# Kernel optimization log

Measured on AMD Instinct MI355X. Metric: run time of the kernel, lower is better.

## Reference

```python
import jax, jax.numpy as jnp
import numpy as np

S, B, DIM = 1024, 4, 768
N_EXPERTS = 8
# hidden_dim = 256 * ceil(int(2*4*dim/3)/256) = 2048 for dim=768
HID = 2048


def setup_inputs() -> dict:
    key = jax.random.key(0)
    ks = jax.random.split(key, 6)
    scale = 0.02
    return {
        "hidden_states": jax.random.normal(ks[0], (S, B, DIM), dtype=jnp.float32),
        "router_w": jax.random.normal(ks[1], (DIM, N_EXPERTS), dtype=jnp.float32) * scale,
        "router_b": jnp.zeros((N_EXPERTS,), dtype=jnp.float32),
        "w1": jax.random.normal(ks[2], (N_EXPERTS, DIM, HID), dtype=jnp.float32) * scale,
        "w2": jax.random.normal(ks[3], (N_EXPERTS, DIM, HID), dtype=jnp.float32) * scale,
        "w3": jax.random.normal(ks[4], (N_EXPERTS, HID, DIM), dtype=jnp.float32) * scale,
    }


def reference(hidden_states, router_w, router_b, w1, w2, w3):
    s, b, h = hidden_states.shape
    # top-1 router
    route = jax.nn.softmax(hidden_states @ router_w + router_b, axis=2)  # [s,b,E]
    max_prob = jnp.max(route, axis=2).reshape(-1, 1)   # [T,1]
    max_ind = jnp.argmax(route, axis=2).reshape(-1)    # [T]
    x = hidden_states.reshape(-1, h)                   # [T,d]

    out = jnp.zeros_like(x)
    # fixed small loop over experts; masked dispatch (tokens not routed to e
    # are zeroed so they contribute nothing)
    for e in range(N_EXPERTS):
        mask = (max_ind == e)[:, None]                 # [T,1]
        xe = jnp.where(mask, x, 0.0)
        oe = (jax.nn.silu(xe @ w1[e]) * (xe @ w2[e])) @ w3[e]
        out = out + jnp.where(mask, oe, 0.0)

    # original stores expert outputs in a bf16 buffer before the prob combine
    out = out.astype(jnp.bfloat16) * max_prob          # bf16 * f32 -> f32
    return out.reshape(s, b, h)
```

## Files before the change

kernel.cpp:

```cpp
#include <hip/hip_runtime.h>


#define T_TOK 4096
#define DIM   768
#define HID   2048
#define NE    8
#define ECAP  1024

#define KB1 24
#define NB1 128
#define KB2 64
#define NB2 48
#define MBC 64

typedef _Float16 f16x8 __attribute__((ext_vector_type(8)));
typedef float    f32x4 __attribute__((ext_vector_type(4)));

#define AS1 __attribute__((address_space(1)))
#define AS3 __attribute__((address_space(3)))

__device__ __forceinline__ void gload_lds16(const _Float16* g, _Float16* l) {
    __builtin_amdgcn_global_load_lds((const AS1 unsigned int*)g,
                                     (AS3 unsigned int*)l, 16, 0, 0);
}

__device__ __forceinline__ float bf16_rne(float v) {
    unsigned u = __float_as_uint(v);
    unsigned r = (u + 0x7fffu + ((u >> 16) & 1u)) & 0xffff0000u;
    return __uint_as_float(r);
}

__device__ __forceinline__ void convert_tile(
    const float* __restrict__ src, _Float16* __restrict__ dst,
    float* Lt, int N, int KBc, int ngrp, int kgrp)
{
    const int t  = threadIdx.x;
    const int c4 = (t & 31) * 4;
    const int r0 = (t >> 5) * 8;
    const float* p = src + (size_t)(kgrp * 64 + r0) * N + ngrp * 128 + c4;
    float4 v[8];
#pragma unroll
    for (int j = 0; j < 8; ++j) v[j] = *(const float4*)(p + (size_t)j * N);
#pragma unroll
    for (int j = 0; j < 8; ++j) {
        float* row = &Lt[(r0 + j) * 130 + c4];
        *(float2*)(row)     = make_float2(v[j].x, v[j].y);
        *(float2*)(row + 2) = make_float2(v[j].z, v[j].w);
    }
    __syncthreads();

    const int l = t & 63, w = t >> 6;
    const int fr = l & 15, fq = l >> 4;
#pragma unroll
    for (int i = 0; i < 4; ++i) {
        const int cell = w * 4 + i;
        const int kbl = cell >> 3, nbl = cell & 7;
        f16x8 h;
#pragma unroll
        for (int j = 0; j < 8; ++j)
            h[j] = (_Float16)Lt[(kbl * 32 + fq * 8 + j) * 130 + nbl * 16 + fr];
        const int nb = ngrp * 8 + nbl, kb = kgrp * 2 + kbl;
        *(f16x8*)(dst + ((size_t)nb * KBc + kb) * 512 + l * 8) = h;
    }
}

__global__ __launch_bounds__(256) void moe_convert_w1_kernel(
    const float* __restrict__ w1, _Float16* __restrict__ w1s)
{
    __shared__ float Lt[64 * 130];
    const int e = blockIdx.x / 192, tile = blockIdx.x % 192;
    convert_tile(w1 + (size_t)e * DIM * HID, w1s + (size_t)e * NB1 * KB1 * 512,
                 Lt, HID, KB1, tile & 15, tile >> 4);
}

__global__ __launch_bounds__(256) void moe_convert_w2_kernel(
    const float* __restrict__ w2, _Float16* __restrict__ w2s)
{
    __shared__ float Lt[64 * 130];
    const int e = blockIdx.x / 192, tile = blockIdx.x % 192;
    convert_tile(w2 + (size_t)e * DIM * HID, w2s + (size_t)e * NB1 * KB1 * 512,
                 Lt, HID, KB1, tile & 15, tile >> 4);
}

__global__ __launch_bounds__(256) void moe_convert_w3_kernel(
    const float* __restrict__ w3, _Float16* __restrict__ w3s)
{
    __shared__ float Lt[64 * 130];
    const int e = blockIdx.x / 192, tile = blockIdx.x % 192;
    convert_tile(w3 + (size_t)e * HID * DIM, w3s + (size_t)e * NB2 * KB2 * 512,
                 Lt, DIM, KB2, tile % 6, tile / 6);
}

__global__ __launch_bounds__(256) void moe_router_kernel(
    const float* __restrict__ X, const float* __restrict__ rw,
    const float* __restrict__ rb, float* __restrict__ probs,
    int* __restrict__ maxind)
{
    const int t = blockIdx.x * 4 + (threadIdx.x >> 6);
    const int l = threadIdx.x & 63;
    const int e = l >> 3;
    const int g = l & 7;
    const float* x = X + (size_t)t * DIM + g * 96;
    const float* w = rw + e;

    double s0 = 0.0, s1 = 0.0;
#pragma unroll
    for (int j4 = 0; j4 < 24; ++j4) {
        const float4 xv = *(const float4*)(x + j4 * 4);
        const int d = (g * 96 + j4 * 4) * NE;
        s0 += (double)xv.x * (double)w[d];
        s1 += (double)xv.y * (double)w[d + NE];
        s0 += (double)xv.z * (double)w[d + 2 * NE];
        s1 += (double)xv.w * (double)w[d + 3 * NE];
    }
    double s = s0 + s1;
    s += __shfl_xor(s, 1, 64);
    s += __shfl_xor(s, 2, 64);
    s += __shfl_xor(s, 4, 64);
    s += (double)rb[e];

    double m = s; int mi = e;
#pragma unroll
    for (int o = 8; o <= 32; o <<= 1) {
        const double om = __shfl_xor(m, o, 64);
        const int   omi = __shfl_xor(mi, o, 64);
        if (om > m || (om == m && omi < mi)) { m = om; mi = omi; }
    }
    float ex = __expf((float)(s - m));
#pragma unroll
    for (int o = 8; o <= 32; o <<= 1) ex += __shfl_xor(ex, o, 64);

    if (l == 0) { probs[t] = 1.0f / ex; maxind[t] = mi; }
}

__global__ __launch_bounds__(256) void moe_lists_kernel(
    const int* __restrict__ maxind, int* __restrict__ counts,
    int* __restrict__ lists)
{
    const int e = blockIdx.x;
    const int tid = threadIdx.x, wid = tid >> 6, lane = tid & 63;
    __shared__ int wsum[4];
    int* dst = lists + e * T_TOK;
    int base = 0;
    for (int t0 = 0; t0 < T_TOK; t0 += 256) {
        const int t = t0 + tid;
        const bool pred = (maxind[t] == e);
        const unsigned long long bal = __ballot(pred);
        const int prefix = __popcll(bal & ((1ull << lane) - 1ull));
        if (lane == 0) wsum[wid] = __popcll(bal);
        __syncthreads();
        int woff = 0;
#pragma unroll
        for (int w2 = 0; w2 < 4; ++w2)
            if (w2 < wid) woff += wsum[w2];
        const int tot = wsum[0] + wsum[1] + wsum[2] + wsum[3];
        if (pred) dst[base + woff + prefix] = t;
        base += tot;
        __syncthreads();
    }
    if (tid == 0) counts[e] = base;
}

__global__ __launch_bounds__(256) void moe_gather_kernel(
    const float* __restrict__ X, const int* __restrict__ lists,
    const int* __restrict__ counts, _Float16* __restrict__ Ag)
{
    const int e = blockIdx.z;
    int cnt = counts[e]; if (cnt > ECAP) cnt = ECAP;
    const int mgrp = blockIdx.y;
    if (mgrp * 64 >= ((cnt + 63) & ~63)) return;
    const int t = threadIdx.x, w = t >> 6, l = t & 63;
    const int mb = mgrp * 4 + w;
    const int m  = mb * 16 + (l & 15);
    const bool valid = (m < cnt);
    const int tok = valid ? lists[e * T_TOK + m] : 0;
    const float* xr = X + (size_t)tok * DIM + (l >> 4) * 8;
#pragma unroll
    for (int i = 0; i < 4; ++i) {
        const int kb = blockIdx.x * 4 + i;
        float4 a = make_float4(0.f, 0.f, 0.f, 0.f), b = a;
        if (valid) {
            a = *(const float4*)(xr + kb * 32);
            b = *(const float4*)(xr + kb * 32 + 4);
        }
        f16x8 h;
        h[0] = (_Float16)a.x; h[1] = (_Float16)a.y; h[2] = (_Float16)a.z; h[3] = (_Float16)a.w;
        h[4] = (_Float16)b.x; h[5] = (_Float16)b.y; h[6] = (_Float16)b.z; h[7] = (_Float16)b.w;
        *(f16x8*)(Ag + ((size_t)(e * MBC + mb) * KB1 + kb) * 512 + l * 8) = h;
    }
}

__global__ __launch_bounds__(256, 4) void moe_gemm1_kernel(
    const _Float16* __restrict__ Ag, const _Float16* __restrict__ w1s,
    const _Float16* __restrict__ w2s, const int* __restrict__ counts,
    _Float16* __restrict__ Hs)
{
    const int e = blockIdx.z;
    int cnt = counts[e]; if (cnt > ECAP) cnt = ECAP;
    const int by = blockIdx.y, bx = blockIdx.x;
    if (by * 128 >= cnt) return;
    const int t = threadIdx.x, w = t >> 6, l = t & 63;
    const int wm = w & 1, wn = w >> 1;

    __shared__ _Float16 Ls[2][16 * 512];

    const int c0s = w * 4;
    const _Float16* gsrc[4];
#pragma unroll
    for (int i = 0; i < 4; ++i) {
        const int c = c0s + i;
        if (c < 8)
            gsrc[i] = Ag  + ((size_t)((e * MBC + by * 8 + c) * KB1)) * 512;
        else if (c < 12)
            gsrc[i] = w1s + ((size_t)((e * NB1 + bx * 4 + (c - 8)) * KB1)) * 512;
        else
            gsrc[i] = w2s + ((size_t)((e * NB1 + bx * 4 + (c - 12)) * KB1)) * 512;
        gsrc[i] += (size_t)l * 8;
    }

    f32x4 acc1[4][2], acc2[4][2];
    const f32x4 zero = {0.f, 0.f, 0.f, 0.f};
#pragma unroll
    for (int i = 0; i < 4; ++i)
#pragma unroll
        for (int j = 0; j < 2; ++j) { acc1[i][j] = zero; acc2[i][j] = zero; }

    auto STAGE = [&](int kb, _Float16* Lb) {
#pragma unroll
        for (int i = 0; i < 4; ++i)
            gload_lds16(gsrc[i] + (size_t)kb * 512, Lb + (c0s + i) * 512);
    };

    STAGE(0, &Ls[0][0]);
    __syncthreads();
    for (int kb = 0; kb < KB1; ++kb) {
        _Float16* Lb = &Ls[kb & 1][0];
        if (kb + 1 < KB1) STAGE(kb + 1, &Ls[(kb + 1) & 1][0]);

        f16x8 a[4], p[2], q[2];
#pragma unroll
        for (int i = 0; i < 4; ++i)
            a[i] = *(const f16x8*)(Lb + (wm * 4 + i) * 512 + l * 8);
#pragma unroll
        for (int j = 0; j < 2; ++j) {
            p[j] = *(const f16x8*)(Lb + (8  + wn * 2 + j) * 512 + l * 8);
            q[j] = *(const f16x8*)(Lb + (12 + wn * 2 + j) * 512 + l * 8);
        }
#pragma unroll
        for (int i = 0; i < 4; ++i)
#pragma unroll
            for (int j = 0; j < 2; ++j) {
                acc1[i][j] = __builtin_amdgcn_mfma_f32_16x16x32_f16(a[i], p[j], acc1[i][j], 0, 0, 0);
                acc2[i][j] = __builtin_amdgcn_mfma_f32_16x16x32_f16(a[i], q[j], acc2[i][j], 0, 0, 0);
            }
        __syncthreads();
    }

    _Float16* Ep = &Ls[0][0] + (size_t)w * (64 * 40);
    const int fq = l >> 4, fr = l & 15;
#pragma unroll
    for (int i = 0; i < 4; ++i)
#pragma unroll
        for (int j = 0; j < 2; ++j)
#pragma unroll
            for (int r = 0; r < 4; ++r) {
                const float h1 = acc1[i][j][r], h2 = acc2[i][j][r];
                const float s  = h1 / (1.f + __expf(-h1)) * h2;
                Ep[(i * 16 + fq * 4 + r) * 40 + j * 16 + fr] = (_Float16)s;
            }
    __syncthreads();
    const int kbH = bx * 2 + wn;
#pragma unroll
    for (int i = 0; i < 4; ++i) {
        f16x8 v = *(const f16x8*)&Ep[(i * 16 + fr) * 40 + fq * 8];
        *(f16x8*)(Hs + ((size_t)((e * MBC + by * 8 + wm * 4 + i) * KB2 + kbH)) * 512 + l * 8) = v;
    }
}

__global__ __launch_bounds__(256, 4) void moe_gemm2_kernel(
    const _Float16* __restrict__ Hs, const _Float16* __restrict__ w3s,
    const int* __restrict__ lists, const int* __restrict__ counts,
    const float* __restrict__ probs, float* __restrict__ out)
{
    const int e = blockIdx.z;
    int cnt = counts[e]; if (cnt > ECAP) cnt = ECAP;
    const int by = blockIdx.y, bx = blockIdx.x;
    if (by * 64 >= cnt) return;
    const int t = threadIdx.x, w = t >> 6, l = t & 63;

    __shared__ _Float16 La[2][8 * 512];

    const _Float16* Asrc = Hs + ((size_t)((e * MBC + by * 4 + w) * KB2)) * 512 + l * 8;
    const int nb0 = e * NB2 + bx * 8 + w * 2;
    const _Float16* Bb = w3s + ((size_t)nb0 * KB2) * 512 + l * 8;

    f32x4 acc[4][2];
    const f32x4 zero = {0.f, 0.f, 0.f, 0.f};
#pragma unroll
    for (int i = 0; i < 4; ++i) { acc[i][0] = zero; acc[i][1] = zero; }

    f16x8 vB0[4], vB1[4];

    auto STAGE_A = [&](int s, _Float16* Lb) {
        gload_lds16(Asrc + (size_t)(2 * s)     * 512, Lb +      w  * 512);
        gload_lds16(Asrc + (size_t)(2 * s + 1) * 512, Lb + (4 + w) * 512);
    };
    auto GB = [&](f16x8* vB, int s) {
#pragma unroll
        for (int u = 0; u < 2; ++u)
#pragma unroll
            for (int j = 0; j < 2; ++j)
                vB[u * 2 + j] = *(const f16x8*)(Bb + ((size_t)(j * KB2 + 2 * s + u)) * 512);
    };
    auto STEP = [&](int s, const f16x8* curB, f16x8* nxtB,
                    _Float16* Lb, _Float16* Ln) {
        if (s + 1 < KB2 / 2) { STAGE_A(s + 1, Ln); GB(nxtB, s + 1); }
#pragma unroll
        for (int u = 0; u < 2; ++u) {
            f16x8 a[4];
#pragma unroll
            for (int i = 0; i < 4; ++i)
                a[i] = *(const f16x8*)(Lb + (u * 4 + i) * 512 + l * 8);
#pragma unroll
            for (int i = 0; i < 4; ++i)
#pragma unroll
                for (int j = 0; j < 2; ++j)
                    acc[i][j] = __builtin_amdgcn_mfma_f32_16x16x32_f16(a[i], curB[u * 2 + j], acc[i][j], 0, 0, 0);
        }
        __syncthreads();
    };

    STAGE_A(0, &La[0][0]); GB(vB0, 0);
    __syncthreads();
    for (int s2 = 0; s2 < KB2 / 2; s2 += 2) {
        STEP(s2,     vB0, vB1, &La[0][0], &La[1][0]);
        STEP(s2 + 1, vB1, vB0, &La[1][0], &La[0][0]);
    }

    const int* list = lists + e * T_TOK;
    const int fq = l >> 4, fr = l & 15;
    const int c0 = bx * 128 + w * 32;
#pragma unroll
    for (int i = 0; i < 4; ++i)
#pragma unroll
        for (int r = 0; r < 4; ++r) {
            const int m = by * 64 + i * 16 + fq * 4 + r;
            if (m < cnt) {
                const int tok = list[m];
                const float pb = probs[tok];
                float* orow = out + (size_t)tok * DIM + c0 + fr;
                orow[0]  = bf16_rne(acc[i][0][r]) * pb;
                orow[16] = bf16_rne(acc[i][1][r]) * pb;
            }
        }
}

extern "C" void kernel_launch(void* const* d_in, const int* in_sizes, int n_in,
                              void* d_out, int out_size, void* d_ws, size_t ws_size,
                              hipStream_t stream) {
    const float* X  = (const float*)d_in[0];
    const float* rw = (const float*)d_in[1];
    const float* rb = (const float*)d_in[2];
    const float* w1 = (const float*)d_in[3];
    const float* w2 = (const float*)d_in[4];
    const float* w3 = (const float*)d_in[5];
    float* out = (float*)d_out;

    char* ws = (char*)d_ws;
    int*      counts = (int*)(ws + 0);
    int*      lists  = (int*)(ws + 256);
    float*    probs  = (float*)(ws + 131328);
    const size_t WSZ = 25165824;
    _Float16* w1s = (_Float16*)(ws + 147712);
    _Float16* w2s = (_Float16*)(ws + 147712 + WSZ);
    _Float16* w3s = (_Float16*)(ws + 147712 + 2 * WSZ);
    _Float16* Ag  = (_Float16*)(ws + 147712 + 3 * WSZ);
    _Float16* Hs  = (_Float16*)(ws + 147712 + 3 * WSZ + 12582912);
    int* maxind = (int*)Ag;

    hipLaunchKernelGGL(moe_convert_w1_kernel, dim3(1536), dim3(256), 0, stream, w1, w1s);
    hipLaunchKernelGGL(moe_convert_w2_kernel, dim3(1536), dim3(256), 0, stream, w2, w2s);
    hipLaunchKernelGGL(moe_convert_w3_kernel, dim3(1536), dim3(256), 0, stream, w3, w3s);
    hipLaunchKernelGGL(moe_router_kernel, dim3(T_TOK / 4), dim3(256), 0, stream,
                       X, rw, rb, probs, maxind);
    hipLaunchKernelGGL(moe_lists_kernel, dim3(NE), dim3(256), 0, stream,
                       maxind, counts, lists);
    hipLaunchKernelGGL(moe_gather_kernel, dim3(6, 16, 8), dim3(256), 0, stream,
                       X, lists, counts, Ag);
    hipLaunchKernelGGL(moe_gemm1_kernel, dim3(32, 8, 8), dim3(256), 0, stream,
                       Ag, w1s, w2s, counts, Hs);
    hipLaunchKernelGGL(moe_gemm2_kernel, dim3(6, 16, 8), dim3(256), 0, stream,
                       Hs, w3s, lists, counts, probs, out);
}
```

Measured before the change: 304.5 us.

## Load gate/up weight fragments straight to registers in gemm1, staging only activations in LDS

The first expert GEMM now stages only the activation tiles through LDS. The w1/w2 weight fragments are read directly from global memory into double-buffered registers, one k-step ahead of the MFMA work. The epilogue scratch gets its own LDS array instead of aliasing the staging buffer. The aim is to cut LDS write/read traffic and LDS footprint for the B operands. In exchange, the two waves sharing a weight column both fetch it from global memory, so weight traffic doubles, and register pressure rises.

```diff
diff --git a/kernel.cpp b/kernel.cpp
--- a/kernel.cpp
+++ b/kernel.cpp
@@ -202,21 +202,14 @@
     const int t = threadIdx.x, w = t >> 6, l = t & 63;
     const int wm = w & 1, wn = w >> 1;
 
-    __shared__ _Float16 Ls[2][16 * 512];
-
-    const int c0s = w * 4;
-    const _Float16* gsrc[4];
-#pragma unroll
-    for (int i = 0; i < 4; ++i) {
-        const int c = c0s + i;
-        if (c < 8)
-            gsrc[i] = Ag  + ((size_t)((e * MBC + by * 8 + c) * KB1)) * 512;
-        else if (c < 12)
-            gsrc[i] = w1s + ((size_t)((e * NB1 + bx * 4 + (c - 8)) * KB1)) * 512;
-        else
-            gsrc[i] = w2s + ((size_t)((e * NB1 + bx * 4 + (c - 12)) * KB1)) * 512;
-        gsrc[i] += (size_t)l * 8;
-    }
+    __shared__ _Float16 Ls[2][8 * 512];
+    __shared__ _Float16 Ep[4][64 * 40];
+
+    const _Float16* Asrc0 = Ag + ((size_t)((e * MBC + by * 8 + 2 * w)     * KB1)) * 512 + l * 8;
+    const _Float16* Asrc1 = Ag + ((size_t)((e * MBC + by * 8 + 2 * w + 1) * KB1)) * 512 + l * 8;
+    const int nb0 = e * NB1 + bx * 4 + wn * 2;
+    const _Float16* B1b = w1s + ((size_t)nb0 * KB1) * 512 + l * 8;
+    const _Float16* B2b = w2s + ((size_t)nb0 * KB1) * 512 + l * 8;
 
     f32x4 acc1[4][2], acc2[4][2];
     const f32x4 zero = {0.f, 0.f, 0.f, 0.f};
@@ -225,38 +218,47 @@
 #pragma unroll
         for (int j = 0; j < 2; ++j) { acc1[i][j] = zero; acc2[i][j] = zero; }
 
-    auto STAGE = [&](int kb, _Float16* Lb) {
-#pragma unroll
-        for (int i = 0; i < 4; ++i)
-            gload_lds16(gsrc[i] + (size_t)kb * 512, Lb + (c0s + i) * 512);
-    };
-
-    STAGE(0, &Ls[0][0]);
-    __syncthreads();
-    for (int kb = 0; kb < KB1; ++kb) {
+    f16x8 p0[2], q0[2], p1[2], q1[2];
+
+    auto STAGE_A = [&](int kb, _Float16* Lb) {
+        gload_lds16(Asrc0 + (size_t)kb * 512, Lb + (2 * w)     * 512);
+        gload_lds16(Asrc1 + (size_t)kb * 512, Lb + (2 * w + 1) * 512);
+    };
+    auto GB = [&](f16x8* p, f16x8* q, int kb) {
+#pragma unroll
+        for (int j = 0; j < 2; ++j) {
+            p[j] = *(const f16x8*)(B1b + ((size_t)(j * KB1 + kb)) * 512);
+            q[j] = *(const f16x8*)(B2b + ((size_t)(j * KB1 + kb)) * 512);
+        }
+    };
+    auto STEP = [&](int kb, const f16x8* cp, const f16x8* cq,
+                    f16x8* np, f16x8* nq) {
         _Float16* Lb = &Ls[kb & 1][0];
-        if (kb + 1 < KB1) STAGE(kb + 1, &Ls[(kb + 1) & 1][0]);
-
-        f16x8 a[4], p[2], q[2];
+        if (kb + 1 < KB1) {
+            STAGE_A(kb + 1, &Ls[(kb + 1) & 1][0]);
+            GB(np, nq, kb + 1);
+        }
+        f16x8 a[4];
 #pragma unroll
         for (int i = 0; i < 4; ++i)
             a[i] = *(const f16x8*)(Lb + (wm * 4 + i) * 512 + l * 8);
 #pragma unroll
-        for (int j = 0; j < 2; ++j) {
-            p[j] = *(const f16x8*)(Lb + (8  + wn * 2 + j) * 512 + l * 8);
-            q[j] = *(const f16x8*)(Lb + (12 + wn * 2 + j) * 512 + l * 8);
-        }
-#pragma unroll
         for (int i = 0; i < 4; ++i)
 #pragma unroll
             for (int j = 0; j < 2; ++j) {
-                acc1[i][j] = __builtin_amdgcn_mfma_f32_16x16x32_f16(a[i], p[j], acc1[i][j], 0, 0, 0);
-                acc2[i][j] = __builtin_amdgcn_mfma_f32_16x16x32_f16(a[i], q[j], acc2[i][j], 0, 0, 0);
+                acc1[i][j] = __builtin_amdgcn_mfma_f32_16x16x32_f16(a[i], cp[j], acc1[i][j], 0, 0, 0);
+                acc2[i][j] = __builtin_amdgcn_mfma_f32_16x16x32_f16(a[i], cq[j], acc2[i][j], 0, 0, 0);
             }
         __syncthreads();
-    }
-
-    _Float16* Ep = &Ls[0][0] + (size_t)w * (64 * 40);
+    };
+
+    STAGE_A(0, &Ls[0][0]); GB(p0, q0, 0);
+    __syncthreads();
+    for (int kb = 0; kb < KB1; kb += 2) {
+        STEP(kb,     p0, q0, p1, q1);
+        STEP(kb + 1, p1, q1, p0, q0);
+    }
+
     const int fq = l >> 4, fr = l & 15;
 #pragma unroll
     for (int i = 0; i < 4; ++i)
@@ -266,13 +268,13 @@
             for (int r = 0; r < 4; ++r) {
                 const float h1 = acc1[i][j][r], h2 = acc2[i][j][r];
                 const float s  = h1 / (1.f + __expf(-h1)) * h2;
-                Ep[(i * 16 + fq * 4 + r) * 40 + j * 16 + fr] = (_Float16)s;
+                Ep[w][(i * 16 + fq * 4 + r) * 40 + j * 16 + fr] = (_Float16)s;
             }
     __syncthreads();
     const int kbH = bx * 2 + wn;
 #pragma unroll
     for (int i = 0; i < 4; ++i) {
-        f16x8 v = *(const f16x8*)&Ep[(i * 16 + fr) * 40 + fq * 8];
+        f16x8 v = *(const f16x8*)&Ep[w][(i * 16 + fr) * 40 + fq * 8];
         *(f16x8*)(Hs + ((size_t)((e * MBC + by * 8 + wm * 4 + i) * KB2 + kbH)) * 512 + l * 8) = v;
     }
 }
```

Measured after the change: 314.8 us. +3.4%, slower.
